# Performance work log

Measured on AMD Instinct MI355X. Metric: run time of the kernel, lower is better.

## Reference

```python
import jax, jax.numpy as jnp
import numpy as np

B, N, D, E, L = 8, 4096, 256, 65536, 1  # graphs, padded nodes, d_model, padded edges, num_layers


def setup_inputs() -> dict:
    key = jax.random.key(0)
    ks = jax.random.split(key, 9)
    x = jax.random.normal(ks[0], (B, N, D), dtype=jnp.float32)
    edge_index = jax.random.randint(ks[1], (B, 2, E), 0, N)
    edge_weight = jax.random.uniform(ks[2], (B, E), dtype=jnp.float32)
    mask = jax.random.randint(ks[3], (B, N), 0, 2).astype(jnp.int32)
    s = 1.0 / np.sqrt(D)
    # GatedGraphConv per-layer linear weight [L, D, D]
    W = jax.random.uniform(ks[4], (L, D, D), jnp.float32, -s, s)
    # GRUCell parameters (r, z, n stacked)
    W_ih = jax.random.uniform(ks[5], (3 * D, D), jnp.float32, -s, s)
    W_hh = jax.random.uniform(ks[6], (3 * D, D), jnp.float32, -s, s)
    b_ih = jax.random.uniform(ks[7], (3 * D,), jnp.float32, -s, s)
    b_hh = jax.random.uniform(ks[8], (3 * D,), jnp.float32, -s, s)
    return {"x": x, "edge_index": edge_index, "edge_weight": edge_weight,
            "mask": mask, "W": W, "W_ih": W_ih, "W_hh": W_hh,
            "b_ih": b_ih, "b_hh": b_hh}


def _gated_graph_conv(x, u, v, ew, W, W_ih, W_hh, b_ih, b_hh):
    """x:[B,N,D]; u,v:[B,E] src/dst indices; ew:[B,E] (already masked)."""
    h = x
    for l in range(L):
        m = jnp.einsum('bnd,de->bne', h, W[l])            # linear transform
        msg = jnp.take_along_axis(m, u[..., None], axis=1) * ew[..., None]  # [B,E,D]
        agg = jax.vmap(lambda ms, vi: jax.ops.segment_sum(ms, vi, num_segments=N))(msg, v)
        # GRUCell(input=agg, hidden=h)
        gi = agg @ W_ih.T + b_ih                          # [B,N,3D]
        gh = h @ W_hh.T + b_hh
        r = jax.nn.sigmoid(gi[..., :D] + gh[..., :D])
        z = jax.nn.sigmoid(gi[..., D:2 * D] + gh[..., D:2 * D])
        n = jnp.tanh(gi[..., 2 * D:] + r * gh[..., 2 * D:])
        h = (1.0 - z) * n + z * h
    return h


def reference(x, edge_index, edge_weight, mask, W, W_ih, W_hh, b_ih, b_hh):
    node_valid = mask > 0                                  # [B,N]
    u = edge_index[:, 0]                                   # source
    v = edge_index[:, 1]                                   # target
    # Drop edges touching invalid nodes: weight -> 0 (equivalent under sum aggr)
    e_valid = jnp.take_along_axis(node_valid, u, axis=1) & jnp.take_along_axis(node_valid, v, axis=1)
    ew = edge_weight * e_valid.astype(edge_weight.dtype)
    h = _gated_graph_conv(x, u, v, ew, W, W_ih, W_hh, b_ih, b_hh)
    # Invalid nodes stay zero (original writes only valid rows of a zeros output)
    return h * node_valid[..., None].astype(h.dtype)
```

## Files before the change

kernel.cpp:

```cpp
#include <hip/hip_runtime.h>
#include <math.h>

#define Bn 8
#define Nn 4096
#define Dn 256
#define En 65536
#define CAP 48

typedef __bf16 bf8 __attribute__((ext_vector_type(8)));
typedef float f4 __attribute__((ext_vector_type(4)));
typedef unsigned short us8 __attribute__((ext_vector_type(8)));

__device__ __forceinline__ float4 ld4(const float* p) { return *(const float4*)p; }

__device__ __forceinline__ unsigned short f2bf(float f) {
    union { float f; unsigned int u; } v; v.f = f;
    unsigned int r = v.u + 0x7fff + ((v.u >> 16) & 1);
    return (unsigned short)(r >> 16);
}
__device__ __forceinline__ float bf2f(unsigned short h) {
    union { unsigned int u; float f; } v; v.u = (unsigned int)h << 16;
    return v.f;
}


__device__ __forceinline__ void stage16c(const unsigned short* __restrict__ gchunk,
                                         int stride, char* ldschunk, int lane) {
    int u = lane >> 3, s = lane & 7;
    int xx = s ^ (u & 7);
    const unsigned short* g = gchunk + (size_t)(2 * u + (xx >> 2)) * stride + (xx & 3) * 8;
    __builtin_amdgcn_global_load_lds((const __attribute__((address_space(1))) void*)g,
                                     (__attribute__((address_space(3))) void*)ldschunk,
                                     16, 0, 0);
}

__device__ __forceinline__ bf8 fragld(const unsigned short* region, int r, int q) {
    int s = (((r & 1) << 2) | q) ^ ((r >> 1) & 7);
    return *(const bf8*)(region + (r >> 1) * 64 + s * 8);
}

__device__ __forceinline__ void ldswrite8(unsigned short* region, int r, int q,
                                          const unsigned short* vals) {
    int s = (((r & 1) << 2) | q) ^ ((r >> 1) & 7);
    *(us8*)(region + (r >> 1) * 64 + s * 8) = *(const us8*)vals;
}


__device__ void rowscan_piece(const int* __restrict__ mask, int* __restrict__ rowidx,
                              int* __restrict__ rowcnt, int* part) {
    int t = threadIdx.x;
    int base = t * 128;
    unsigned long long b0 = 0, b1 = 0;
    int s = 0;
#pragma unroll 8
    for (int i = 0; i < 64; i++) {
        int m = mask[base + i] > 0;
        b0 |= (unsigned long long)m << i; s += m;
    }
#pragma unroll 8
    for (int i = 0; i < 64; i++) {
        int m = mask[base + 64 + i] > 0;
        b1 |= (unsigned long long)m << i; s += m;
    }
    part[t] = s;
    __syncthreads();
    for (int st = 1; st < 256; st <<= 1) {
        int v = (t >= st) ? part[t - st] : 0;
        __syncthreads();
        part[t] += v;
        __syncthreads();
    }
    int run = part[t] - s;
    for (int i = 0; i < 64; i++)
        if ((b0 >> i) & 1) rowidx[run++] = base + i;
    for (int i = 0; i < 64; i++)
        if ((b1 >> i) & 1) rowidx[run++] = base + 64 + i;
    if (t == 255) rowcnt[0] = part[255];
}

__device__ void wf_piece(int wfi, const float* __restrict__ Wih, const float* __restrict__ W,
                         unsigned short* __restrict__ Ball, unsigned short* lds) {
    int t = threadIdx.x, lane = t & 63, w = t >> 6;
    int wr = w >> 1, wc = w & 1, q = lane >> 4, c16 = lane & 15;
    int o0 = (wfi % 6) * 128, d0b = (wfi / 6) * 64;
    f4 acc[4][2];
    f4 zz = {0.f, 0.f, 0.f, 0.f};
#pragma unroll
    for (int rt = 0; rt < 4; rt++)
#pragma unroll
        for (int ct = 0; ct < 2; ct++) acc[rt][ct] = zz;

    int r = t >> 1, half = t & 1;
    for (int k0 = 0; k0 < 256; k0 += 32) {
        const float* pa = Wih + (size_t)(o0 + r) * 256 + k0 + half * 16;
        float4 a0 = ld4(pa), a1 = ld4(pa + 4), a2 = ld4(pa + 8), a3 = ld4(pa + 12);
        float4 b0, b1, b2, b3;
        if (t < 128) {
            const float* pb = W + (size_t)(d0b + r) * 256 + k0 + half * 16;
            b0 = ld4(pb); b1 = ld4(pb + 4); b2 = ld4(pb + 8); b3 = ld4(pb + 12);
        }
        __syncthreads();
        unsigned short tmp[16];
        tmp[0] = f2bf(a0.x); tmp[1] = f2bf(a0.y); tmp[2] = f2bf(a0.z); tmp[3] = f2bf(a0.w);
        tmp[4] = f2bf(a1.x); tmp[5] = f2bf(a1.y); tmp[6] = f2bf(a1.z); tmp[7] = f2bf(a1.w);
        tmp[8] = f2bf(a2.x); tmp[9] = f2bf(a2.y); tmp[10] = f2bf(a2.z); tmp[11] = f2bf(a2.w);
        tmp[12] = f2bf(a3.x); tmp[13] = f2bf(a3.y); tmp[14] = f2bf(a3.z); tmp[15] = f2bf(a3.w);
        ldswrite8(lds, r, half * 2, tmp);
        ldswrite8(lds, r, half * 2 + 1, tmp + 8);
        if (t < 128) {
            unsigned short tb[16];
            tb[0] = f2bf(b0.x); tb[1] = f2bf(b0.y); tb[2] = f2bf(b0.z); tb[3] = f2bf(b0.w);
            tb[4] = f2bf(b1.x); tb[5] = f2bf(b1.y); tb[6] = f2bf(b1.z); tb[7] = f2bf(b1.w);
            tb[8] = f2bf(b2.x); tb[9] = f2bf(b2.y); tb[10] = f2bf(b2.z); tb[11] = f2bf(b2.w);
            tb[12] = f2bf(b3.x); tb[13] = f2bf(b3.y); tb[14] = f2bf(b3.z); tb[15] = f2bf(b3.w);
            ldswrite8(lds + 4096, r, half * 2, tb);
            ldswrite8(lds + 4096, r, half * 2 + 1, tb + 8);
        }
        __syncthreads();
        bf8 a[4];
#pragma unroll
        for (int rt = 0; rt < 4; rt++) a[rt] = fragld(lds, wr * 64 + rt * 16 + c16, q);
#pragma unroll
        for (int ct = 0; ct < 2; ct++) {
            bf8 b = fragld(lds + 4096, wc * 32 + ct * 16 + c16, q);
#pragma unroll
            for (int rt = 0; rt < 4; rt++)
                acc[rt][ct] = __builtin_amdgcn_mfma_f32_16x16x32_bf16(a[rt], b, acc[rt][ct], 0, 0, 0);
        }
    }
#pragma unroll
    for (int ct = 0; ct < 2; ct++) {
        int col = d0b + wc * 32 + ct * 16 + c16;
#pragma unroll
        for (int rt = 0; rt < 4; rt++) {
            int ob = o0 + wr * 64 + rt * 16 + q * 4;
#pragma unroll
            for (int i = 0; i < 4; i++)
                Ball[(size_t)(ob + i) * 512 + col] = f2bf(acc[rt][ct][i]);
        }
    }
}

__global__ __launch_bounds__(256) void setup_kernel(const int* __restrict__ ei,
                                                    const int* __restrict__ mask,
                                                    const float* __restrict__ Wih,
                                                    const float* __restrict__ W,
                                                    const float* __restrict__ Whh,
                                                    const float* __restrict__ ew,
                                                    int* __restrict__ cnt,
                                                    int2* __restrict__ bucket,
                                                    int* __restrict__ rowidx,
                                                    int* __restrict__ rowcnt,
                                                    unsigned short* __restrict__ Ball,
                                                    float* __restrict__ out) {
    __shared__ __align__(16) unsigned short lds[6144];
    int b = blockIdx.x, t = threadIdx.x;
    if (b == 0) {
        rowscan_piece(mask, rowidx, rowcnt, (int*)lds);
        return;
    }
    if (b < 25) {
        wf_piece(b - 1, Wih, W, Ball, lds);
        return;
    }
    if (b < 217) {
        int i = ((b - 25) * 256 + t) * 4;
        float4 wv = ld4(Whh + i);
        int o = i >> 8, d = i & 255;
        ushort4 ov;
        ov.x = f2bf(wv.x); ov.y = f2bf(wv.y); ov.z = f2bf(wv.z); ov.w = f2bf(wv.w);
        *(ushort4*)(Ball + (size_t)o * 512 + 256 + d) = ov;
        return;
    }
    if (b < 2265) {
        int idx = (b - 217) * 256 + t;
        int bb = idx >> 16, e = idx & 65535;
        const int* eb = ei + (size_t)bb * 2 * En;
        int u = eb[e];
        int v = eb[En + e];
        const int* mb = mask + bb * Nn;
        if (mb[u] > 0 && mb[v] > 0) {
            int pos = atomicAdd(&cnt[bb * Nn + v], 1);
            if (pos < CAP) {
                int2 pr;
                pr.x = u;
                pr.y = __float_as_int(ew[(size_t)bb * En + e]);
                bucket[(size_t)(bb * Nn + v) * CAP + pos] = pr;
            }
        }
        return;
    }
    {
        int zb = b - 2265;
        int r = zb * 8 + (t >> 5);
        if (mask[r] > 0) return;
        int col = (t & 31) * 8;
        float4 z = make_float4(0.f, 0.f, 0.f, 0.f);
        *(float4*)(out + (size_t)r * 256 + col) = z;
        *(float4*)(out + (size_t)r * 256 + col + 4) = z;
    }
}


__global__ __launch_bounds__(256) void agg_kernel(const float* __restrict__ x,
                                                  const int* __restrict__ cnt,
                                                  const int2* __restrict__ bucket,
                                                  const int* __restrict__ rowidx,
                                                  const int* __restrict__ rowcnt,
                                                  unsigned short* __restrict__ Ac) {
    int wave = threadIdx.x >> 6, lane = threadIdx.x & 63;
    int i = blockIdx.x * 4 + wave;
    if (i >= rowcnt[0]) return;
    int v = rowidx[i];
    int b = v >> 12, n = v & 4095;
    int m = cnt[b * Nn + n];
    m = m < CAP ? m : CAP;
    const int2* bk = bucket + (size_t)(b * Nn + n) * CAP;
    const float* Xb = x + (size_t)b * Nn * 256;
    float a0 = 0.f, a1 = 0.f, a2 = 0.f, a3 = 0.f;
    for (int j = 0; j < m; j += 8) {
        int u[8]; float wv[8];
#pragma unroll
        for (int k = 0; k < 8; k++) {
            int jj = j + k;
            bool ok = jj < m;
            int2 pr = bk[ok ? jj : 0];
            u[k] = pr.x;
            wv[k] = ok ? __int_as_float(pr.y) : 0.f;
        }
        float4 mv[8];
#pragma unroll
        for (int k = 0; k < 8; k++) mv[k] = ld4(Xb + (size_t)u[k] * 256 + lane * 4);
#pragma unroll
        for (int k = 0; k < 8; k++) {
            a0 += wv[k] * mv[k].x; a1 += wv[k] * mv[k].y;
            a2 += wv[k] * mv[k].z; a3 += wv[k] * mv[k].w;
        }
    }
    ushort4 o;
    o.x = f2bf(a0); o.y = f2bf(a1); o.z = f2bf(a2); o.w = f2bf(a3);
    *(ushort4*)(Ac + (size_t)i * 512 + lane * 4) = o;
    float4 xv = ld4(x + (size_t)v * 256 + lane * 4);
    ushort4 xo;
    xo.x = f2bf(xv.x); xo.y = f2bf(xv.y); xo.z = f2bf(xv.z); xo.w = f2bf(xv.w);
    *(ushort4*)(Ac + (size_t)i * 512 + 256 + lane * 4) = xo;
}


#define GRU_STAGE(kk, bufbase)                                                      \
    {                                                                               \
        if (w < 4) {                                                                \
            _Pragma("unroll") for (int j = 0; j < 3; j++) {                         \
                int c = w * 3 + j;                                                  \
                const unsigned short* src;                                          \
                if (c < 8)                                                          \
                    src = Ac + (size_t)(row0 + c * 16) * 512 + (kk) * 32;           \
                else {                                                              \
                    int g = (c - 8) >> 2, cg = (c - 8) & 3;                         \
                    src = Ball + (size_t)(g * 256 + d0 + cg * 16) * 512 + (kk) * 32;\
                }                                                                   \
                stage16c(src, 512, (char*)(bufbase) + c * 1024, lane);              \
            }                                                                       \
        } else {                                                                    \
            _Pragma("unroll") for (int j = 0; j < 2; j++) {                         \
                int c = 12 + (w - 4) * 2 + j;                                       \
                int g = (c - 8) >> 2, cg = (c - 8) & 3;                             \
                const unsigned short* src =                                         \
                    Ball + (size_t)(g * 256 + d0 + cg * 16) * 512 + (kk) * 32;      \
                stage16c(src, 512, (char*)(bufbase) + c * 1024, lane);              \
            }                                                                       \
        }                                                                           \
    }

#define GRU_COMPUTE(bufbase, ACCM)                                                  \
    {                                                                               \
        const unsigned short* rb = (bufbase);                                       \
        bf8 a0 = fragld(rb + (wr * 2) * 512, c16, q);                               \
        bf8 a1 = fragld(rb + (wr * 2 + 1) * 512, c16, q);                           \
        _Pragma("unroll") for (int ct = 0; ct < 2; ct++) {                          \
            int cg = wc * 2 + ct;                                                   \
            bf8 br = fragld(rb + (8 + cg) * 512, c16, q);                           \
            bf8 bz = fragld(rb + (12 + cg) * 512, c16, q);                          \
            bf8 bm = fragld(rb + (16 + cg) * 512, c16, q);                          \
            acc_r[0][ct] = __builtin_amdgcn_mfma_f32_16x16x32_bf16(a0, br, acc_r[0][ct], 0, 0, 0); \
            acc_r[1][ct] = __builtin_amdgcn_mfma_f32_16x16x32_bf16(a1, br, acc_r[1][ct], 0, 0, 0); \
            acc_z[0][ct] = __builtin_amdgcn_mfma_f32_16x16x32_bf16(a0, bz, acc_z[0][ct], 0, 0, 0); \
            acc_z[1][ct] = __builtin_amdgcn_mfma_f32_16x16x32_bf16(a1, bz, acc_z[1][ct], 0, 0, 0); \
            ACCM[0][ct] = __builtin_amdgcn_mfma_f32_16x16x32_bf16(a0, bm, ACCM[0][ct], 0, 0, 0);   \
            ACCM[1][ct] = __builtin_amdgcn_mfma_f32_16x16x32_bf16(a1, bm, ACCM[1][ct], 0, 0, 0);   \
        }                                                                           \
    }

__global__ __launch_bounds__(512, 4) void gru_kernel(const unsigned short* __restrict__ Ac,
                                                     const unsigned short* __restrict__ Ball,
                                                     const float* __restrict__ bih,
                                                     const float* __restrict__ bhh,
                                                     const int* __restrict__ rowidx,
                                                     const int* __restrict__ rowcnt,
                                                     float* __restrict__ out) {
    __shared__ __align__(16) unsigned short lds[20480];
    const int t = threadIdx.x;
    const int lane = t & 63, w = t >> 6;
    const int wr = w >> 1, wc = w & 1;
    const int q = lane >> 4, c16 = lane & 15;
    const int row0 = blockIdx.x * 128, d0 = blockIdx.y * 64;
    const int cnt = rowcnt[0];
    if (row0 >= cnt) return;

    f4 acc_r[2][2], acc_z[2][2], acc_gn[2][2], acc_hn[2][2];
    f4 zz = {0.f, 0.f, 0.f, 0.f};
#pragma unroll
    for (int rt = 0; rt < 2; rt++)
#pragma unroll
        for (int ct = 0; ct < 2; ct++) {
            acc_r[rt][ct] = zz; acc_z[rt][ct] = zz;
            acc_gn[rt][ct] = zz; acc_hn[rt][ct] = zz;
        }

    unsigned short* buf0 = lds;
    unsigned short* buf1 = lds + 10240;

    GRU_STAGE(0, buf0)
#pragma unroll
    for (int kk = 0; kk < 8; kk++) {
        __syncthreads();
        GRU_STAGE(kk + 1, (kk & 1) ? buf0 : buf1)
        GRU_COMPUTE((kk & 1) ? buf1 : buf0, acc_gn)
    }
#pragma unroll
    for (int kk = 8; kk < 16; kk++) {
        __syncthreads();
        if (kk < 15) GRU_STAGE(kk + 1, (kk & 1) ? buf0 : buf1)
        GRU_COMPUTE((kk & 1) ? buf1 : buf0, acc_hn)
    }

#pragma unroll
    for (int ct = 0; ct < 2; ct++) {
        int dd = d0 + wc * 32 + ct * 16 + c16;
        float b_r = bih[dd] + bhh[dd];
        float b_z = bih[dd + 256] + bhh[dd + 256];
        float b_gn = bih[dd + 512];
        float b_hn = bhh[dd + 512];
#pragma unroll
        for (int rt = 0; rt < 2; rt++) {
            int rbase = row0 + wr * 32 + rt * 16 + q * 4;
#pragma unroll
            for (int i = 0; i < 4; i++) {
                int rc = rbase + i;
                if (rc < cnt) {
                    float sr = acc_r[rt][ct][i] + b_r;
                    float sz = acc_z[rt][ct][i] + b_z;
                    float gn = acc_gn[rt][ct][i] + b_gn;
                    float hn = acc_hn[rt][ct][i] + b_hn;
                    float rg = 1.f / (1.f + __expf(-sr));
                    float zg = 1.f / (1.f + __expf(-sz));
                    float pre = gn + rg * hn;
                    float e2 = __expf(2.f * pre);
                    float ng = 1.f - 2.f / (e2 + 1.f);
                    float xv = bf2f(Ac[(size_t)rc * 512 + 256 + dd]);
                    float h = (1.f - zg) * ng + zg * xv;
                    int v = rowidx[rc];
                    out[(size_t)v * 256 + dd] = h;
                }
            }
        }
    }
}


extern "C" void kernel_launch(void* const* d_in, const int* in_sizes, int n_in,
                              void* d_out, int out_size, void* d_ws, size_t ws_size,
                              hipStream_t stream) {
    const float* x   = (const float*)d_in[0];
    const int*   ei  = (const int*)d_in[1];
    const float* ew  = (const float*)d_in[2];
    const int*   msk = (const int*)d_in[3];
    const float* W   = (const float*)d_in[4];
    const float* Wih = (const float*)d_in[5];
    const float* Whh = (const float*)d_in[6];
    const float* bih = (const float*)d_in[7];
    const float* bhh = (const float*)d_in[8];
    float* out = (float*)d_out;

    char* p = (char*)d_ws;
    unsigned short* Ac   = (unsigned short*)p; p += (size_t)Bn * Nn * 512 * 2;
    unsigned short* Ball = (unsigned short*)p; p += (size_t)768 * 512 * 2;
    int2* bucket = (int2*)p;  p += (size_t)Bn * Nn * CAP * sizeof(int2);
    int* cnt    = (int*)p;    p += (size_t)Bn * Nn * sizeof(int);
    int* rowidx = (int*)p;    p += (size_t)Bn * Nn * sizeof(int);
    int* rowcnt = (int*)p;    p += 128;

    hipMemsetAsync(cnt, 0, (size_t)Bn * Nn * sizeof(int), stream);
    setup_kernel<<<6361, 256, 0, stream>>>(ei, msk, Wih, W, Whh, ew, cnt, bucket,
                                           rowidx, rowcnt, Ball, out);
    agg_kernel<<<(Bn * Nn) / 4, 256, 0, stream>>>(x, cnt, bucket, rowidx, rowcnt, Ac);
    gru_kernel<<<dim3(256, 4), 512, 0, stream>>>(Ac, Ball, bih, bhh, rowidx, rowcnt, out);
}
```

Baseline: 178.3 us.

## Triple-buffer GRU GEMM staging with explicit vmcnt waits and priority

Replaces the double-buffered LDS pipeline in the GRU kernel with a three-buffer scheme that prefetches two k-steps ahead. It uses manual s_waitcnt vmcnt counts per wave group and raw s_barrier calls instead of __syncthreads, plus s_setprio around the MFMA compute. The aim is to hide global load latency behind the matrix math. In exchange it raises LDS use by half, which may lower occupancy, and it relies on the hand-counted vmcnt values matching the number of loads each wave issues.

```diff
diff --git a/kernel.cpp b/kernel.cpp
--- a/kernel.cpp
+++ b/kernel.cpp
@@ -291,6 +291,30 @@
         }                                                                           \
     }
 
+#define GRU_WAITV(n04, n47)                                                         \
+    if (w < 4) { asm volatile("s_waitcnt vmcnt(" #n04 ")" ::: "memory"); }          \
+    else       { asm volatile("s_waitcnt vmcnt(" #n47 ")" ::: "memory"); }          \
+    __builtin_amdgcn_sched_barrier(0);
+
+#define GRU_STEP(kk, STAGEBUF, COMPBUF, ACCM, n04, n47)                             \
+    __builtin_amdgcn_s_barrier();             \
+    GRU_STAGE((kk) + 2, STAGEBUF)                                                   \
+    GRU_WAITV(n04, n47)                             \
+    __builtin_amdgcn_s_barrier();                   \
+    __builtin_amdgcn_s_setprio(1);                                                  \
+    GRU_COMPUTE(COMPBUF, ACCM)                                                      \
+    __builtin_amdgcn_s_setprio(0);                                                  \
+    __builtin_amdgcn_sched_barrier(0);
+
+#define GRU_STEP_LAST(kk, COMPBUF, ACCM, n04, n47)                                  \
+    __builtin_amdgcn_s_barrier();                                                   \
+    GRU_WAITV(n04, n47)                                                             \
+    __builtin_amdgcn_s_barrier();                                                   \
+    __builtin_amdgcn_s_setprio(1);                                                  \
+    GRU_COMPUTE(COMPBUF, ACCM)                                                      \
+    __builtin_amdgcn_s_setprio(0);                                                  \
+    __builtin_amdgcn_sched_barrier(0);
+
 __global__ __launch_bounds__(512, 4) void gru_kernel(const unsigned short* __restrict__ Ac,
                                                      const unsigned short* __restrict__ Ball,
                                                      const float* __restrict__ bih,
@@ -298,7 +322,7 @@
                                                      const int* __restrict__ rowidx,
                                                      const int* __restrict__ rowcnt,
                                                      float* __restrict__ out) {
-    __shared__ __align__(16) unsigned short lds[20480];
+    __shared__ __align__(16) unsigned short lds[30720];
     const int t = threadIdx.x;
     const int lane = t & 63, w = t >> 6;
     const int wr = w >> 1, wc = w & 1;
@@ -317,22 +341,29 @@
             acc_gn[rt][ct] = zz; acc_hn[rt][ct] = zz;
         }
 
-    unsigned short* buf0 = lds;
-    unsigned short* buf1 = lds + 10240;
-
-    GRU_STAGE(0, buf0)
-#pragma unroll
-    for (int kk = 0; kk < 8; kk++) {
-        __syncthreads();
-        GRU_STAGE(kk + 1, (kk & 1) ? buf0 : buf1)
-        GRU_COMPUTE((kk & 1) ? buf1 : buf0, acc_gn)
-    }
-#pragma unroll
-    for (int kk = 8; kk < 16; kk++) {
-        __syncthreads();
-        if (kk < 15) GRU_STAGE(kk + 1, (kk & 1) ? buf0 : buf1)
-        GRU_COMPUTE((kk & 1) ? buf1 : buf0, acc_hn)
-    }
+    unsigned short* bufA = lds;
+    unsigned short* bufB = lds + 10240;
+    unsigned short* bufC = lds + 20480;
+
+    GRU_STAGE(0, bufA)
+    GRU_STAGE(1, bufB)
+
+    GRU_STEP(0,  bufC, bufA, acc_gn, 6, 4)
+    GRU_STEP(1,  bufA, bufB, acc_gn, 6, 4)
+    GRU_STEP(2,  bufB, bufC, acc_gn, 6, 4)
+    GRU_STEP(3,  bufC, bufA, acc_gn, 6, 4)
+    GRU_STEP(4,  bufA, bufB, acc_gn, 6, 4)
+    GRU_STEP(5,  bufB, bufC, acc_gn, 6, 4)
+    GRU_STEP(6,  bufC, bufA, acc_gn, 6, 4)
+    GRU_STEP(7,  bufA, bufB, acc_gn, 6, 4)
+    GRU_STEP(8,  bufB, bufC, acc_hn, 6, 4)
+    GRU_STEP(9,  bufC, bufA, acc_hn, 6, 4)
+    GRU_STEP(10, bufA, bufB, acc_hn, 6, 4)
+    GRU_STEP(11, bufB, bufC, acc_hn, 6, 4)
+    GRU_STEP(12, bufC, bufA, acc_hn, 6, 4)
+    GRU_STEP(13, bufA, bufB, acc_hn, 6, 4)
+    GRU_STEP_LAST(14, bufC, acc_hn, 3, 2)
+    GRU_STEP_LAST(15, bufA, acc_hn, 0, 0)
 
 #pragma unroll
     for (int ct = 0; ct < 2; ct++) {
```

Measured after the change: 166.1 us. -6.8%, faster.

## Shrink GRU tile to 64 rows and restructure staging pipeline with explicit waits

Applied to the files above, without the earlier changes.

The GRU GEMM block shrinks from 128 rows/512 threads to 64 rows/256 threads, doubling the grid and lowering LDS use. This should allow more resident blocks per CU. The k-loop is merged into one loop using raw s_barrier, explicit vmcnt waits so the next stage's loads overlap compute, and setprio around the MFMA section. The agg kernel also issues the self-feature load early to hide its latency. Risks include halved B-tile reuse per block and depending on the vmcnt count matching what stage16c actually issues.

```diff
diff --git a/kernel.cpp b/kernel.cpp
--- a/kernel.cpp
+++ b/kernel.cpp
@@ -213,6 +213,7 @@
     if (i >= rowcnt[0]) return;
     int v = rowidx[i];
     int b = v >> 12, n = v & 4095;
+    float4 xv = ld4(x + (size_t)v * 256 + lane * 4);
     int m = cnt[b * Nn + n];
     m = m < CAP ? m : CAP;
     const int2* bk = bucket + (size_t)(b * Nn + n) * CAP;
@@ -240,7 +241,6 @@
     ushort4 o;
     o.x = f2bf(a0); o.y = f2bf(a1); o.z = f2bf(a2); o.w = f2bf(a3);
     *(ushort4*)(Ac + (size_t)i * 512 + lane * 4) = o;
-    float4 xv = ld4(x + (size_t)v * 256 + lane * 4);
     ushort4 xo;
     xo.x = f2bf(xv.x); xo.y = f2bf(xv.y); xo.z = f2bf(xv.z); xo.w = f2bf(xv.w);
     *(ushort4*)(Ac + (size_t)i * 512 + 256 + lane * 4) = xo;
@@ -249,26 +249,16 @@
 
 #define GRU_STAGE(kk, bufbase)                                                      \
     {                                                                               \
-        if (w < 4) {                                                                \
-            _Pragma("unroll") for (int j = 0; j < 3; j++) {                         \
-                int c = w * 3 + j;                                                  \
-                const unsigned short* src;                                          \
-                if (c < 8)                                                          \
-                    src = Ac + (size_t)(row0 + c * 16) * 512 + (kk) * 32;           \
-                else {                                                              \
-                    int g = (c - 8) >> 2, cg = (c - 8) & 3;                         \
-                    src = Ball + (size_t)(g * 256 + d0 + cg * 16) * 512 + (kk) * 32;\
-                }                                                                   \
-                stage16c(src, 512, (char*)(bufbase) + c * 1024, lane);              \
+        _Pragma("unroll") for (int j = 0; j < 4; j++) {                             \
+            int c = w * 4 + j;                                                      \
+            const unsigned short* src;                                              \
+            if (c < 4)                                                              \
+                src = Ac + (size_t)(row0 + c * 16) * 512 + (kk) * 32;               \
+            else {                                                                  \
+                int g = (c - 4) >> 2, cg = (c - 4) & 3;                             \
+                src = Ball + (size_t)(g * 256 + d0 + cg * 16) * 512 + (kk) * 32;    \
             }                                                                       \
-        } else {                                                                    \
-            _Pragma("unroll") for (int j = 0; j < 2; j++) {                         \
-                int c = 12 + (w - 4) * 2 + j;                                       \
-                int g = (c - 8) >> 2, cg = (c - 8) & 3;                             \
-                const unsigned short* src =                                         \
-                    Ball + (size_t)(g * 256 + d0 + cg * 16) * 512 + (kk) * 32;      \
-                stage16c(src, 512, (char*)(bufbase) + c * 1024, lane);              \
-            }                                                                       \
+            stage16c(src, 512, (char*)(bufbase) + c * 1024, lane);                  \
         }                                                                           \
     }
 
@@ -279,9 +269,9 @@
         bf8 a1 = fragld(rb + (wr * 2 + 1) * 512, c16, q);                           \
         _Pragma("unroll") for (int ct = 0; ct < 2; ct++) {                          \
             int cg = wc * 2 + ct;                                                   \
-            bf8 br = fragld(rb + (8 + cg) * 512, c16, q);                           \
-            bf8 bz = fragld(rb + (12 + cg) * 512, c16, q);                          \
-            bf8 bm = fragld(rb + (16 + cg) * 512, c16, q);                          \
+            bf8 br = fragld(rb + (4 + cg) * 512, c16, q);                           \
+            bf8 bz = fragld(rb + (8 + cg) * 512, c16, q);                           \
+            bf8 bm = fragld(rb + (12 + cg) * 512, c16, q);                          \
             acc_r[0][ct] = __builtin_amdgcn_mfma_f32_16x16x32_bf16(a0, br, acc_r[0][ct], 0, 0, 0); \
             acc_r[1][ct] = __builtin_amdgcn_mfma_f32_16x16x32_bf16(a1, br, acc_r[1][ct], 0, 0, 0); \
             acc_z[0][ct] = __builtin_amdgcn_mfma_f32_16x16x32_bf16(a0, bz, acc_z[0][ct], 0, 0, 0); \
@@ -291,19 +281,19 @@
         }                                                                           \
     }
 
-__global__ __launch_bounds__(512, 4) void gru_kernel(const unsigned short* __restrict__ Ac,
+__global__ __launch_bounds__(256, 5) void gru_kernel(const unsigned short* __restrict__ Ac,
                                                      const unsigned short* __restrict__ Ball,
                                                      const float* __restrict__ bih,
                                                      const float* __restrict__ bhh,
                                                      const int* __restrict__ rowidx,
                                                      const int* __restrict__ rowcnt,
                                                      float* __restrict__ out) {
-    __shared__ __align__(16) unsigned short lds[20480];
+    __shared__ __align__(16) unsigned short lds[16384];
     const int t = threadIdx.x;
     const int lane = t & 63, w = t >> 6;
     const int wr = w >> 1, wc = w & 1;
     const int q = lane >> 4, c16 = lane & 15;
-    const int row0 = blockIdx.x * 128, d0 = blockIdx.y * 64;
+    const int row0 = blockIdx.x * 64, d0 = blockIdx.y * 64;
     const int cnt = rowcnt[0];
     if (row0 >= cnt) return;
 
@@ -318,20 +308,28 @@
         }
 
     unsigned short* buf0 = lds;
-    unsigned short* buf1 = lds + 10240;
+    unsigned short* buf1 = lds + 8192;
 
     GRU_STAGE(0, buf0)
 #pragma unroll
-    for (int kk = 0; kk < 8; kk++) {
-        __syncthreads();
-        GRU_STAGE(kk + 1, (kk & 1) ? buf0 : buf1)
-        GRU_COMPUTE((kk & 1) ? buf1 : buf0, acc_gn)
-    }
-#pragma unroll
-    for (int kk = 8; kk < 16; kk++) {
-        __syncthreads();
-        if (kk < 15) GRU_STAGE(kk + 1, (kk & 1) ? buf0 : buf1)
-        GRU_COMPUTE((kk & 1) ? buf1 : buf0, acc_hn)
+    for (int kk = 0; kk < 16; kk++) {
+        unsigned short* sbuf = (kk & 1) ? buf0 : buf1;
+        unsigned short* cbuf = (kk & 1) ? buf1 : buf0;
+        __builtin_amdgcn_s_barrier();
+        if (kk < 15) {
+            GRU_STAGE(kk + 1, sbuf)
+            asm volatile("s_waitcnt vmcnt(4)" ::: "memory");
+        } else {
+            asm volatile("s_waitcnt vmcnt(0)" ::: "memory");
+        }
+        __builtin_amdgcn_sched_barrier(0);
+        __builtin_amdgcn_s_barrier();
+        __builtin_amdgcn_sched_barrier(0);
+        __builtin_amdgcn_s_setprio(1);
+        if (kk < 8) { GRU_COMPUTE(cbuf, acc_gn) }
+        else        { GRU_COMPUTE(cbuf, acc_hn) }
+        __builtin_amdgcn_s_setprio(0);
+        __builtin_amdgcn_sched_barrier(0);
     }
 
 #pragma unroll
@@ -394,5 +392,5 @@
     setup_kernel<<<6361, 256, 0, stream>>>(ei, msk, Wih, W, Whh, ew, cnt, bucket,
                                            rowidx, rowcnt, Ball, out);
     agg_kernel<<<(Bn * Nn) / 4, 256, 0, stream>>>(x, cnt, bucket, rowidx, rowcnt, Ac);
-    gru_kernel<<<dim3(256, 4), 512, 0, stream>>>(Ac, Ball, bih, bhh, rowidx, rowcnt, out);
-}
+    gru_kernel<<<dim3(512, 4), 256, 0, stream>>>(Ac, Ball, bih, bhh, rowidx, rowcnt, out);
+}
```

Result: faster. 170.6 us (-4.4%).
